# Optimization experiments

Hardware: AMD Instinct MI355X
Metric: run time of the kernel (lower is better)

The kernel has to match this reference:

```python
import jax, jax.numpy as jnp
import numpy as np

DEPTH = 7  # complete binary trees with 2**DEPTH = 128 leaves

B, L = 4096, 128
V, E, OUT = 100000, 128, 3


def setup_inputs() -> dict:
    key = jax.random.key(0)
    ks = jax.random.split(key, 6)
    tokens = jax.random.randint(ks[0], (B, L), 0, V, dtype=jnp.int64)
    embedding = jax.random.normal(ks[1], (V, E), dtype=jnp.float32)
    # tree_layer: Linear(2E -> E); torch stores weight as [out, in]
    W_tree = jax.random.normal(ks[2], (E, 2 * E), dtype=jnp.float32) * (1.0 / np.sqrt(2 * E))
    b_tree = jax.random.normal(ks[3], (E,), dtype=jnp.float32) * 0.01
    # classifier_layer: Linear(E -> OUT)
    W_cls = jax.random.normal(ks[4], (OUT, E), dtype=jnp.float32) * (1.0 / np.sqrt(E))
    b_cls = jax.random.normal(ks[5], (OUT,), dtype=jnp.float32) * 0.01
    return {"tokens": tokens, "embedding": embedding, "W_tree": W_tree,
            "b_tree": b_tree, "W_cls": W_cls, "b_cls": b_cls}


def reference(tokens, embedding, W_tree, b_tree, W_cls, b_cls):
    # Leaf embeddings: gather rows of the embedding table. [B, L, E]
    reps = embedding[tokens]
    # Level-synchronous bottom-up composition (depth-batched across all trees):
    # at each level, pair adjacent nodes, concat features, apply tree_layer + tanh.
    for _ in range(DEPTH):
        left = reps[:, 0::2, :]   # [B, n/2, E]
        right = reps[:, 1::2, :]  # [B, n/2, E]
        combined = jnp.concatenate([left, right], axis=-1)  # [B, n/2, 2E]
        reps = jnp.tanh(jnp.einsum('bnh,eh->bne', combined, W_tree) + b_tree)
    roots = reps[:, 0, :]  # [B, E]
    return roots @ W_cls.T + b_cls  # [B, OUT]
```

## Files before the change

### kernel.cpp

```cpp
#include <hip/hip_runtime.h>
#include <hip/hip_fp16.h>


typedef _Float16 half8 __attribute__((ext_vector_type(8)));
typedef float floatx4 __attribute__((ext_vector_type(4)));

#define STRIDE 264
#define UROW   33
#define NPAIR  2048

__device__ __forceinline__ float fast_tanh(float x) {
  float e = __expf(2.f * x);
  return 1.f - 2.f * __builtin_amdgcn_rcpf(e + 1.f);
}

__device__ __forceinline__ unsigned pkrtz(float a, float b) {
  auto h = __builtin_amdgcn_cvt_pkrtz(a, b);
  return __builtin_bit_cast(unsigned, h);
}

__device__ __forceinline__ void load16(const float* __restrict__ emb, int tok, int seg,
                                       float4 (&st)[16]) {
  const float4* src = (const float4*)emb + (size_t)tok * 32 + (seg & 1) * 16;
#pragma unroll
  for (int j = 0; j < 16; ++j) st[j] = src[j];
}
__device__ __forceinline__ void cvt_write(const float4 (&st)[16], _Float16* buf,
                                          int row, int seg) {
  uint4* dst = (uint4*)buf + row * UROW + seg * 8;
#pragma unroll
  for (int j = 0; j < 8; ++j) {
    float4 x = st[2 * j], y = st[2 * j + 1];
    uint4 w;
    w.x = pkrtz(x.x, x.y); w.y = pkrtz(x.z, x.w);
    w.z = pkrtz(y.x, y.y); w.w = pkrtz(y.z, y.w);
    dst[j] = w;
  }
}

__device__ __forceinline__ void mfma_k256(const _Float16* arow, const half8 (&Wf)[2][8],
                                          const float (&bias)[2], floatx4 (&accO)[2]) {
  floatx4 aA[2], aB[2];
#pragma unroll
  for (int i = 0; i < 2; ++i) {
    aA[i] = (floatx4){bias[i], bias[i], bias[i], bias[i]};
    aB[i] = (floatx4){0.f, 0.f, 0.f, 0.f};
  }
#pragma unroll
  for (int ks = 0; ks < 4; ++ks) {
    half8 x0 = *(const half8*)(arow + ks * 32);
    half8 x1 = *(const half8*)(arow + (ks + 4) * 32);
    aA[0] = __builtin_amdgcn_mfma_f32_16x16x32_f16(x0, Wf[0][ks],     aA[0], 0, 0, 0);
    aB[0] = __builtin_amdgcn_mfma_f32_16x16x32_f16(x1, Wf[0][ks + 4], aB[0], 0, 0, 0);
    aA[1] = __builtin_amdgcn_mfma_f32_16x16x32_f16(x0, Wf[1][ks],     aA[1], 0, 0, 0);
    aB[1] = __builtin_amdgcn_mfma_f32_16x16x32_f16(x1, Wf[1][ks + 4], aB[1], 0, 0, 0);
  }
  accO[0] = aA[0] + aB[0];
  accO[1] = aA[1] + aB[1];
}

template<int MT, int IN_S, int MVALID>
__device__ __forceinline__ void level_b(const _Float16* inb, _Float16* outb,
                                        const half8 (&Wf)[2][8], const float (&bias)[2],
                                        int nbase, int l15, int quad)
{
#pragma unroll
  for (int m = 0; m < MT; ++m) {
    floatx4 acc[2];
    mfma_k256(inb + (m * 16 + l15) * STRIDE + quad * 8, Wf, bias, acc);
    const int mrow = m * 16 + quad * 4;
#pragma unroll
    for (int i = 0; i < 2; ++i) {
      const int col = (nbase + i) * 16 + l15;
#pragma unroll
      for (int r = 0; r < 4; ++r) {
        const int node = mrow + r;
        if (MVALID == MT * 16 || node < MVALID) {
          const int s  = node / IN_S;
          const int ln = node % IN_S;
          float v = fast_tanh(acc[i][r]);
          outb[((ln >> 1) + s * (IN_S >> 1)) * STRIDE + (ln & 1) * 128 + col] = (_Float16)v;
        }
      }
    }
  }
}

__global__ __launch_bounds__(256, 2)
void tree_kernel(const int* __restrict__ tokens,
                 const float* __restrict__ embedding,
                 const float* __restrict__ W_tree,
                 const float* __restrict__ b_tree,
                 const float* __restrict__ W_cls,
                 const float* __restrict__ b_cls,
                 float* __restrict__ out)
{
  __shared__ __align__(16) _Float16 bufA[64 * STRIDE];
  __shared__ __align__(16) _Float16 bufB[32 * STRIDE];
  __shared__ __align__(16) _Float16 bufD[32 * STRIDE];
  __shared__ float wavepart[4][2][3];

  const int tid  = threadIdx.x;
  const int wid  = tid >> 6;
  const int lane = tid & 63;
  const int l15  = lane & 15;
  const int quad = lane >> 4;
  const int nbase = wid * 2;
  const int row  = tid & 63;
  const int seg  = tid >> 6;
  const int tidx = 2 * row + (seg >> 1);

  half8 Wf[2][8];
#pragma unroll
  for (int i = 0; i < 2; ++i) {
    const int e = (nbase + i) * 16 + l15;
#pragma unroll
    for (int ks = 0; ks < 8; ++ks) {
      const int k = ks * 32 + quad * 8;
      const float4* p = (const float4*)(W_tree + e * 256 + k);
      float4 lo = p[0], hi = p[1];
      half8 f;
      f[0] = (_Float16)lo.x; f[1] = (_Float16)lo.y; f[2] = (_Float16)lo.z; f[3] = (_Float16)lo.w;
      f[4] = (_Float16)hi.x; f[5] = (_Float16)hi.y; f[6] = (_Float16)hi.z; f[7] = (_Float16)hi.w;
      Wf[i][ks] = f;
    }
  }
  float bias[2];
#pragma unroll
  for (int i = 0; i < 2; ++i) bias[i] = b_tree[(nbase + i) * 16 + l15];

  float wc[2][3];
#pragma unroll
  for (int i = 0; i < 2; ++i) {
#pragma unroll
    for (int o = 0; o < 3; ++o) wc[i][o] = W_cls[o * 128 + (nbase + i) * 16 + l15];
  }

  int tokB_cur = tokens[(2 * blockIdx.x + 1) * 128 + tidx];
  {
    const int tokA0 = tokens[(2 * blockIdx.x) * 128 + tidx];
    float4 st[16];
    load16(embedding, tokA0, seg, st);
    cvt_write(st, bufA, row, seg);
  }
  __syncthreads();

#pragma unroll 1
  for (int p = blockIdx.x; p < NPAIR; p += gridDim.x) {
    int pn = p + gridDim.x;
    if (pn >= NPAIR) pn = p;
    const bool first = (p == (int)blockIdx.x);
    const int pprev = p - (int)gridDim.x;
    const int tokA_nxt = tokens[(2 * pn) * 128 + tidx];
    const int tokB_nxt = tokens[(2 * pn + 1) * 128 + tidx];

    if (!first) {
      floatx4 acc[2];
      mfma_k256(bufD + l15 * STRIDE + quad * 8, Wf, bias, acc);
      float part[2][3] = {{0.f, 0.f, 0.f}, {0.f, 0.f, 0.f}};
      if (quad == 0) {
#pragma unroll
        for (int i = 0; i < 2; ++i)
#pragma unroll
          for (int rr = 0; rr < 2; ++rr) {
            float v = fast_tanh(acc[i][rr]);
#pragma unroll
            for (int o = 0; o < 3; ++o) part[rr][o] = fmaf(v, wc[i][o], part[rr][o]);
          }
      }
#pragma unroll
      for (int rr = 0; rr < 2; ++rr)
#pragma unroll
        for (int o = 0; o < 3; ++o) {
          float v = part[rr][o];
          v += __shfl_down(v, 8);
          v += __shfl_down(v, 4);
          v += __shfl_down(v, 2);
          v += __shfl_down(v, 1);
          if (lane == 0) wavepart[wid][rr][o] = v;
        }
    }
    level_b<4, 64, 64>(bufA, bufB, Wf, bias, nbase, l15, quad);
    __syncthreads();

    {
      float4 st[16];
      load16(embedding, tokB_cur, seg, st);
      if (!first && tid < 6) {
        const int rr = tid / 3, o = tid - 3 * rr;
        float v = wavepart[0][rr][o] + wavepart[1][rr][o]
                + wavepart[2][rr][o] + wavepart[3][rr][o];
        out[(2 * pprev + rr) * 3 + o] = v + b_cls[o];
      }
      level_b<2, 32, 32>(bufB, bufD, Wf, bias, nbase, l15, quad);
      cvt_write(st, bufA, row, seg);
    }
    __syncthreads();

    level_b<4, 64, 64>(bufA, bufB, Wf, bias, nbase, l15, quad);
    __syncthreads();

    {
      float4 st[16];
      load16(embedding, tokA_nxt, seg, st);
      level_b<2, 32, 32>(bufB, bufD + 16 * STRIDE, Wf, bias, nbase, l15, quad);
      cvt_write(st, bufA, row, seg);
    }
    __syncthreads();

    level_b<2, 16, 32>(bufD, bufB, Wf, bias, nbase, l15, quad);
    __syncthreads();

    level_b<1, 8, 16>(bufB, bufD, Wf, bias, nbase, l15, quad);
    __syncthreads();

    level_b<1, 4, 8>(bufD, bufB, Wf, bias, nbase, l15, quad);
    __syncthreads();

    level_b<1, 2, 4>(bufB, bufD, Wf, bias, nbase, l15, quad);
    __syncthreads();

    tokB_cur = tokB_nxt;
  }

  {
    const int plast = (int)blockIdx.x + ((NPAIR / 1 - 1 - (int)blockIdx.x) / (int)gridDim.x) * (int)gridDim.x;
    floatx4 acc[2];
    mfma_k256(bufD + l15 * STRIDE + quad * 8, Wf, bias, acc);
    float part[2][3] = {{0.f, 0.f, 0.f}, {0.f, 0.f, 0.f}};
    if (quad == 0) {
#pragma unroll
      for (int i = 0; i < 2; ++i)
#pragma unroll
        for (int rr = 0; rr < 2; ++rr) {
          float v = fast_tanh(acc[i][rr]);
#pragma unroll
          for (int o = 0; o < 3; ++o) part[rr][o] = fmaf(v, wc[i][o], part[rr][o]);
        }
    }
#pragma unroll
    for (int rr = 0; rr < 2; ++rr)
#pragma unroll
      for (int o = 0; o < 3; ++o) {
        float v = part[rr][o];
        v += __shfl_down(v, 8);
        v += __shfl_down(v, 4);
        v += __shfl_down(v, 2);
        v += __shfl_down(v, 1);
        if (lane == 0) wavepart[wid][rr][o] = v;
      }
    __syncthreads();
    if (tid < 6) {
      const int rr = tid / 3, o = tid - 3 * rr;
      float v = wavepart[0][rr][o] + wavepart[1][rr][o]
              + wavepart[2][rr][o] + wavepart[3][rr][o];
      out[(2 * plast + rr) * 3 + o] = v + b_cls[o];
    }
  }
}

extern "C" void kernel_launch(void* const* d_in, const int* in_sizes, int n_in,
                              void* d_out, int out_size, void* d_ws, size_t ws_size,
                              hipStream_t stream) {
  const int*   tokens    = (const int*)d_in[0];
  const float* embedding = (const float*)d_in[1];
  const float* W_tree    = (const float*)d_in[2];
  const float* b_tree    = (const float*)d_in[3];
  const float* W_cls     = (const float*)d_in[4];
  const float* b_cls     = (const float*)d_in[5];
  float* out = (float*)d_out;

  dim3 grid(512), block(256);
  tree_kernel<<<grid, block, 0, stream>>>(tokens, embedding, W_tree, b_tree, W_cls, b_cls, out);
}
```

Before: 164.0 us.

## Double block size to 8 waves splitting M tiles across two wave groups

Grows the block from 4 to 8 waves. The two groups of 4 waves split the row (M) tiles of each tree level, and the embedding gather is spread over twice as many threads in smaller chunks. The root/classifier step runs on the second group while the first group starts the next level. Classifier weights are now loaded on demand rather than held in registers. The goal is more latency hiding and lower per-wave register pressure. The cost is idle waves in the deep levels, where only group 0 works, and launch bounds that may force register spills.

After: 209.6 us. +27.8%, slower.

```diff
diff --git a/kernel.cpp b/kernel.cpp
--- a/kernel.cpp
+++ b/kernel.cpp
@@ -19,17 +19,17 @@
   return __builtin_bit_cast(unsigned, h);
 }
 
-__device__ __forceinline__ void load16(const float* __restrict__ emb, int tok, int seg,
-                                       float4 (&st)[16]) {
-  const float4* src = (const float4*)emb + (size_t)tok * 32 + (seg & 1) * 16;
-#pragma unroll
-  for (int j = 0; j < 16; ++j) st[j] = src[j];
-}
-__device__ __forceinline__ void cvt_write(const float4 (&st)[16], _Float16* buf,
-                                          int row, int seg) {
-  uint4* dst = (uint4*)buf + row * UROW + seg * 8;
-#pragma unroll
-  for (int j = 0; j < 8; ++j) {
+__device__ __forceinline__ void load4(const float* __restrict__ emb, int tok, int seg,
+                                      int b, float4 (&st)[4]) {
+  const float4* src = (const float4*)emb + (size_t)tok * 32 + (seg & 3) * 8 + b * 4;
+#pragma unroll
+  for (int j = 0; j < 4; ++j) st[j] = src[j];
+}
+__device__ __forceinline__ void cvt_write4(const float4 (&st)[4], _Float16* buf,
+                                           int row, int seg, int b) {
+  uint4* dst = (uint4*)buf + row * UROW + (seg >> 2) * 16 + (seg & 3) * 4 + b * 2;
+#pragma unroll
+  for (int j = 0; j < 2; ++j) {
     float4 x = st[2 * j], y = st[2 * j + 1];
     uint4 w;
     w.x = pkrtz(x.x, x.y); w.y = pkrtz(x.z, x.w);
@@ -59,23 +59,23 @@
   accO[1] = aA[1] + aB[1];
 }
 
-template<int MT, int IN_S, int MVALID>
+template<int MT_LOC, int IN_S, int MVALID>
 __device__ __forceinline__ void level_b(const _Float16* inb, _Float16* outb,
                                         const half8 (&Wf)[2][8], const float (&bias)[2],
-                                        int nbase, int l15, int quad)
+                                        int mbase, int nbase, int l15, int quad)
 {
 #pragma unroll
-  for (int m = 0; m < MT; ++m) {
+  for (int m = 0; m < MT_LOC; ++m) {
     floatx4 acc[2];
-    mfma_k256(inb + (m * 16 + l15) * STRIDE + quad * 8, Wf, bias, acc);
-    const int mrow = m * 16 + quad * 4;
+    mfma_k256(inb + ((mbase + m) * 16 + l15) * STRIDE + quad * 8, Wf, bias, acc);
+    const int mrow = (mbase + m) * 16 + quad * 4;
 #pragma unroll
     for (int i = 0; i < 2; ++i) {
       const int col = (nbase + i) * 16 + l15;
 #pragma unroll
       for (int r = 0; r < 4; ++r) {
         const int node = mrow + r;
-        if (MVALID == MT * 16 || node < MVALID) {
+        if (MVALID < 0 || node < MVALID) {
           const int s  = node / IN_S;
           const int ln = node % IN_S;
           float v = fast_tanh(acc[i][r]);
@@ -86,7 +86,7 @@
   }
 }
 
-__global__ __launch_bounds__(256, 2)
+__global__ __launch_bounds__(512, 4)
 void tree_kernel(const int* __restrict__ tokens,
                  const float* __restrict__ embedding,
                  const float* __restrict__ W_tree,
@@ -105,10 +105,12 @@
   const int lane = tid & 63;
   const int l15  = lane & 15;
   const int quad = lane >> 4;
-  const int nbase = wid * 2;
+  const int wn   = wid & 3;
+  const int wm   = wid >> 2;
+  const int nbase = wn * 2;
   const int row  = tid & 63;
   const int seg  = tid >> 6;
-  const int tidx = 2 * row + (seg >> 1);
+  const int tidx = 2 * row + (seg >> 2);
 
   half8 Wf[2][8];
 #pragma unroll
@@ -129,24 +131,19 @@
 #pragma unroll
   for (int i = 0; i < 2; ++i) bias[i] = b_tree[(nbase + i) * 16 + l15];
 
-  float wc[2][3];
-#pragma unroll
-  for (int i = 0; i < 2; ++i) {
-#pragma unroll
-    for (int o = 0; o < 3; ++o) wc[i][o] = W_cls[o * 128 + (nbase + i) * 16 + l15];
-  }
-
   int tokB_cur = tokens[(2 * blockIdx.x + 1) * 128 + tidx];
   {
     const int tokA0 = tokens[(2 * blockIdx.x) * 128 + tidx];
-    float4 st[16];
-    load16(embedding, tokA0, seg, st);
-    cvt_write(st, bufA, row, seg);
+    float4 st0[4], st1[4];
+    load4(embedding, tokA0, seg, 0, st0);
+    load4(embedding, tokA0, seg, 1, st1);
+    cvt_write4(st0, bufA, row, seg, 0);
+    cvt_write4(st1, bufA, row, seg, 1);
   }
   __syncthreads();
 
 #pragma unroll 1
-  for (int p = blockIdx.x; p < NPAIR; p += gridDim.x) {
+  for (int p = blockIdx.x; p < NPAIR; p += (int)gridDim.x) {
     int pn = p + gridDim.x;
     if (pn >= NPAIR) pn = p;
     const bool first = (p == (int)blockIdx.x);
@@ -154,18 +151,114 @@
     const int tokA_nxt = tokens[(2 * pn) * 128 + tidx];
     const int tokB_nxt = tokens[(2 * pn + 1) * 128 + tidx];
 
-    if (!first) {
+    if (wm == 1) {
+      if (!first) {
+        floatx4 acc[2];
+        mfma_k256(bufD + l15 * STRIDE + quad * 8, Wf, bias, acc);
+        float part[2][3] = {{0.f, 0.f, 0.f}, {0.f, 0.f, 0.f}};
+        if (quad == 0) {
+          float wcl[2][3];
+#pragma unroll
+          for (int i = 0; i < 2; ++i)
+#pragma unroll
+            for (int o = 0; o < 3; ++o) wcl[i][o] = W_cls[o * 128 + (nbase + i) * 16 + l15];
+#pragma unroll
+          for (int i = 0; i < 2; ++i)
+#pragma unroll
+            for (int rr = 0; rr < 2; ++rr) {
+              float v = fast_tanh(acc[i][rr]);
+#pragma unroll
+              for (int o = 0; o < 3; ++o) part[rr][o] = fmaf(v, wcl[i][o], part[rr][o]);
+            }
+        }
+#pragma unroll
+        for (int rr = 0; rr < 2; ++rr)
+#pragma unroll
+          for (int o = 0; o < 3; ++o) {
+            float v = part[rr][o];
+            v += __shfl_down(v, 8);
+            v += __shfl_down(v, 4);
+            v += __shfl_down(v, 2);
+            v += __shfl_down(v, 1);
+            if (lane == 0) wavepart[wn][rr][o] = v;
+          }
+      }
+      level_b<2, 64, -1>(bufA, bufB, Wf, bias, 2, nbase, l15, quad);
+    } else {
+      level_b<2, 64, -1>(bufA, bufB, Wf, bias, 0, nbase, l15, quad);
+    }
+    __syncthreads();
+
+    {
+      float4 st0[4];
+      load4(embedding, tokB_cur, seg, 0, st0);
+      __builtin_amdgcn_sched_barrier(0);
+      if (!first && tid < 6) {
+        const int rr = tid / 3, o = tid - 3 * rr;
+        float v = wavepart[0][rr][o] + wavepart[1][rr][o]
+                + wavepart[2][rr][o] + wavepart[3][rr][o];
+        out[(2 * pprev + rr) * 3 + o] = v + b_cls[o];
+      }
+      level_b<1, 32, -1>(bufB, bufD, Wf, bias, wm, nbase, l15, quad);
+      __builtin_amdgcn_sched_barrier(0);
+      float4 st1[4];
+      load4(embedding, tokB_cur, seg, 1, st1);
+      cvt_write4(st0, bufA, row, seg, 0);
+      cvt_write4(st1, bufA, row, seg, 1);
+    }
+    __syncthreads();
+
+    level_b<2, 64, -1>(bufA, bufB, Wf, bias, wm * 2, nbase, l15, quad);
+    __syncthreads();
+
+    {
+      float4 st0[4];
+      load4(embedding, tokA_nxt, seg, 0, st0);
+      __builtin_amdgcn_sched_barrier(0);
+      level_b<1, 32, -1>(bufB, bufD + 16 * STRIDE, Wf, bias, wm, nbase, l15, quad);
+      __builtin_amdgcn_sched_barrier(0);
+      float4 st1[4];
+      load4(embedding, tokA_nxt, seg, 1, st1);
+      cvt_write4(st0, bufA, row, seg, 0);
+      cvt_write4(st1, bufA, row, seg, 1);
+    }
+    __syncthreads();
+
+    level_b<1, 16, -1>(bufD, bufB, Wf, bias, wm, nbase, l15, quad);
+    __syncthreads();
+
+    if (wm == 0) level_b<1, 8, -1>(bufB, bufD, Wf, bias, 0, nbase, l15, quad);
+    __syncthreads();
+
+    if (wm == 0) level_b<1, 4, 8>(bufD, bufB, Wf, bias, 0, nbase, l15, quad);
+    __syncthreads();
+
+    if (wm == 0) level_b<1, 2, 4>(bufB, bufD, Wf, bias, 0, nbase, l15, quad);
+    __syncthreads();
+
+    tokB_cur = tokB_nxt;
+  }
+
+  {
+    const int plast = (int)blockIdx.x
+        + ((NPAIR - 1 - (int)blockIdx.x) / (int)gridDim.x) * (int)gridDim.x;
+    if (wm == 1) {
       floatx4 acc[2];
       mfma_k256(bufD + l15 * STRIDE + quad * 8, Wf, bias, acc);
       float part[2][3] = {{0.f, 0.f, 0.f}, {0.f, 0.f, 0.f}};
       if (quad == 0) {
+        float wcl[2][3];
+#pragma unroll
+        for (int i = 0; i < 2; ++i)
+#pragma unroll
+          for (int o = 0; o < 3; ++o) wcl[i][o] = W_cls[o * 128 + (nbase + i) * 16 + l15];
 #pragma unroll
         for (int i = 0; i < 2; ++i)
 #pragma unroll
           for (int rr = 0; rr < 2; ++rr) {
             float v = fast_tanh(acc[i][rr]);
 #pragma unroll
-            for (int o = 0; o < 3; ++o) part[rr][o] = fmaf(v, wc[i][o], part[rr][o]);
+            for (int o = 0; o < 3; ++o) part[rr][o] = fmaf(v, wcl[i][o], part[rr][o]);
           }
       }
 #pragma unroll
@@ -177,78 +270,9 @@
           v += __shfl_down(v, 4);
           v += __shfl_down(v, 2);
           v += __shfl_down(v, 1);
-          if (lane == 0) wavepart[wid][rr][o] = v;
+          if (lane == 0) wavepart[wn][rr][o] = v;
         }
     }
-    level_b<4, 64, 64>(bufA, bufB, Wf, bias, nbase, l15, quad);
-    __syncthreads();
-
-    {
-      float4 st[16];
-      load16(embedding, tokB_cur, seg, st);
-      if (!first && tid < 6) {
-        const int rr = tid / 3, o = tid - 3 * rr;
-        float v = wavepart[0][rr][o] + wavepart[1][rr][o]
-                + wavepart[2][rr][o] + wavepart[3][rr][o];
-        out[(2 * pprev + rr) * 3 + o] = v + b_cls[o];
-      }
-      level_b<2, 32, 32>(bufB, bufD, Wf, bias, nbase, l15, quad);
-      cvt_write(st, bufA, row, seg);
-    }
-    __syncthreads();
-
-    level_b<4, 64, 64>(bufA, bufB, Wf, bias, nbase, l15, quad);
-    __syncthreads();
-
-    {
-      float4 st[16];
-      load16(embedding, tokA_nxt, seg, st);
-      level_b<2, 32, 32>(bufB, bufD + 16 * STRIDE, Wf, bias, nbase, l15, quad);
-      cvt_write(st, bufA, row, seg);
-    }
-    __syncthreads();
-
-    level_b<2, 16, 32>(bufD, bufB, Wf, bias, nbase, l15, quad);
-    __syncthreads();
-
-    level_b<1, 8, 16>(bufB, bufD, Wf, bias, nbase, l15, quad);
-    __syncthreads();
-
-    level_b<1, 4, 8>(bufD, bufB, Wf, bias, nbase, l15, quad);
-    __syncthreads();
-
-    level_b<1, 2, 4>(bufB, bufD, Wf, bias, nbase, l15, quad);
-    __syncthreads();
-
-    tokB_cur = tokB_nxt;
-  }
-
-  {
-    const int plast = (int)blockIdx.x + ((NPAIR / 1 - 1 - (int)blockIdx.x) / (int)gridDim.x) * (int)gridDim.x;
-    floatx4 acc[2];
-    mfma_k256(bufD + l15 * STRIDE + quad * 8, Wf, bias, acc);
-    float part[2][3] = {{0.f, 0.f, 0.f}, {0.f, 0.f, 0.f}};
-    if (quad == 0) {
-#pragma unroll
-      for (int i = 0; i < 2; ++i)
-#pragma unroll
-        for (int rr = 0; rr < 2; ++rr) {
-          float v = fast_tanh(acc[i][rr]);
-#pragma unroll
-          for (int o = 0; o < 3; ++o) part[rr][o] = fmaf(v, wc[i][o], part[rr][o]);
-        }
-    }
-#pragma unroll
-    for (int rr = 0; rr < 2; ++rr)
-#pragma unroll
-      for (int o = 0; o < 3; ++o) {
-        float v = part[rr][o];
-        v += __shfl_down(v, 8);
-        v += __shfl_down(v, 4);
-        v += __shfl_down(v, 2);
-        v += __shfl_down(v, 1);
-        if (lane == 0) wavepart[wid][rr][o] = v;
-      }
     __syncthreads();
     if (tid < 6) {
       const int rr = tid / 3, o = tid - 3 * rr;
@@ -270,6 +294,6 @@
   const float* b_cls     = (const float*)d_in[5];
   float* out = (float*)d_out;
 
-  dim3 grid(512), block(256);
+  dim3 grid(512), block(512);
   tree_kernel<<<grid, block, 0, stream>>>(tokens, embedding, W_tree, b_tree, W_cls, b_cls, out);
 }
```

## Shrink LDS buffers and halve embedding staging to fit three blocks per CU

Applied to the files above, without the earlier changes.

Replaces the 32-row bufD with a 6-row bufC and restructures the level schedule so both trees of a pair reuse bufA/bufB in place. Embedding loads are split into two 8-float4 halves per thread, which cuts register staging. The classifier weights are now loaded only when used. Together these let launch bounds rise to 3 blocks per CU and the grid grow to 768, trading more barriers and extra level steps for higher occupancy and more latency hiding.

Result: slower. 183.1 us (+11.6%).

```diff
diff --git a/kernel.cpp b/kernel.cpp
--- a/kernel.cpp
+++ b/kernel.cpp
@@ -19,17 +19,17 @@
   return __builtin_bit_cast(unsigned, h);
 }
 
-__device__ __forceinline__ void load16(const float* __restrict__ emb, int tok, int seg,
-                                       float4 (&st)[16]) {
-  const float4* src = (const float4*)emb + (size_t)tok * 32 + (seg & 1) * 16;
-#pragma unroll
-  for (int j = 0; j < 16; ++j) st[j] = src[j];
-}
-__device__ __forceinline__ void cvt_write(const float4 (&st)[16], _Float16* buf,
-                                          int row, int seg) {
-  uint4* dst = (uint4*)buf + row * UROW + seg * 8;
-#pragma unroll
-  for (int j = 0; j < 8; ++j) {
+__device__ __forceinline__ void load8(const float* __restrict__ emb, int tok, int q,
+                                      float4 (&st)[8]) {
+  const float4* src = (const float4*)emb + (size_t)tok * 32 + q * 8;
+#pragma unroll
+  for (int j = 0; j < 8; ++j) st[j] = src[j];
+}
+__device__ __forceinline__ void cvt_write8(const float4 (&st)[8], _Float16* buf,
+                                           int row, int lb, int q) {
+  uint4* dst = (uint4*)buf + row * UROW + lb * 16 + q * 4;
+#pragma unroll
+  for (int j = 0; j < 4; ++j) {
     float4 x = st[2 * j], y = st[2 * j + 1];
     uint4 w;
     w.x = pkrtz(x.x, x.y); w.y = pkrtz(x.z, x.w);
@@ -75,7 +75,7 @@
 #pragma unroll
       for (int r = 0; r < 4; ++r) {
         const int node = mrow + r;
-        if (MVALID == MT * 16 || node < MVALID) {
+        if (MVALID < 0 || node < MVALID) {
           const int s  = node / IN_S;
           const int ln = node % IN_S;
           float v = fast_tanh(acc[i][r]);
@@ -86,7 +86,7 @@
   }
 }
 
-__global__ __launch_bounds__(256, 2)
+__global__ __launch_bounds__(256, 3)
 void tree_kernel(const int* __restrict__ tokens,
                  const float* __restrict__ embedding,
                  const float* __restrict__ W_tree,
@@ -97,7 +97,7 @@
 {
   __shared__ __align__(16) _Float16 bufA[64 * STRIDE];
   __shared__ __align__(16) _Float16 bufB[32 * STRIDE];
-  __shared__ __align__(16) _Float16 bufD[32 * STRIDE];
+  __shared__ __align__(16) _Float16 bufC[6 * STRIDE];
   __shared__ float wavepart[4][2][3];
 
   const int tid  = threadIdx.x;
@@ -106,9 +106,10 @@
   const int l15  = lane & 15;
   const int quad = lane >> 4;
   const int nbase = wid * 2;
-  const int row  = tid & 63;
-  const int seg  = tid >> 6;
-  const int tidx = 2 * row + (seg >> 1);
+  const int gr   = tid & 31;
+  const int glb  = (tid >> 7) & 1;
+  const int gq   = (tid >> 5) & 3;
+  const int li   = 2 * gr + glb;
 
   half8 Wf[2][8];
 #pragma unroll
@@ -129,43 +130,67 @@
 #pragma unroll
   for (int i = 0; i < 2; ++i) bias[i] = b_tree[(nbase + i) * 16 + l15];
 
-  float wc[2][3];
-#pragma unroll
-  for (int i = 0; i < 2; ++i) {
-#pragma unroll
-    for (int o = 0; o < 3; ++o) wc[i][o] = W_cls[o * 128 + (nbase + i) * 16 + l15];
-  }
-
-  int tokB_cur = tokens[(2 * blockIdx.x + 1) * 128 + tidx];
+  int tokS1lo = tokens[(2 * blockIdx.x + 1) * 128 + li];
+  int tokS1hi = tokens[(2 * blockIdx.x + 1) * 128 + 64 + li];
   {
-    const int tokA0 = tokens[(2 * blockIdx.x) * 128 + tidx];
-    float4 st[16];
-    load16(embedding, tokA0, seg, st);
-    cvt_write(st, bufA, row, seg);
+    const int tlo = tokens[(2 * blockIdx.x) * 128 + li];
+    const int thi = tokens[(2 * blockIdx.x) * 128 + 64 + li];
+    float4 st[8];
+    load8(embedding, tlo, gq, st);
+    cvt_write8(st, bufA, gr, glb, gq);
+    load8(embedding, thi, gq, st);
+    cvt_write8(st, bufA, 32 + gr, glb, gq);
   }
   __syncthreads();
 
 #pragma unroll 1
-  for (int p = blockIdx.x; p < NPAIR; p += gridDim.x) {
+  for (int p = blockIdx.x; p < NPAIR; p += (int)gridDim.x) {
     int pn = p + gridDim.x;
     if (pn >= NPAIR) pn = p;
     const bool first = (p == (int)blockIdx.x);
     const int pprev = p - (int)gridDim.x;
-    const int tokA_nxt = tokens[(2 * pn) * 128 + tidx];
-    const int tokB_nxt = tokens[(2 * pn + 1) * 128 + tidx];
+    const int tokN0lo = tokens[(2 * pn) * 128 + li];
+    const int tokN0hi = tokens[(2 * pn) * 128 + 64 + li];
 
     if (!first) {
+      const int rc = l15 < 4 ? l15 : 3;
       floatx4 acc[2];
-      mfma_k256(bufD + l15 * STRIDE + quad * 8, Wf, bias, acc);
+      mfma_k256(bufC + rc * STRIDE + quad * 8, Wf, bias, acc);
+      const int mrow = quad * 4;
+#pragma unroll
+      for (int i = 0; i < 2; ++i) {
+        const int col = (nbase + i) * 16 + l15;
+#pragma unroll
+        for (int r = 0; r < 4; ++r) {
+          const int node = mrow + r;
+          if (node < 4) {
+            float v = fast_tanh(acc[i][r]);
+            bufC[(4 + (node >> 1)) * STRIDE + (node & 1) * 128 + col] = (_Float16)v;
+          }
+        }
+      }
+    }
+    level_b<4, 64, -1>(bufA, bufB, Wf, bias, nbase, l15, quad);
+    __syncthreads();
+
+    if (!first) {
+      const int rc = 4 + (l15 < 2 ? l15 : 1);
+      floatx4 acc[2];
+      mfma_k256(bufC + rc * STRIDE + quad * 8, Wf, bias, acc);
       float part[2][3] = {{0.f, 0.f, 0.f}, {0.f, 0.f, 0.f}};
       if (quad == 0) {
+        float wcl[2][3];
+#pragma unroll
+        for (int i = 0; i < 2; ++i)
+#pragma unroll
+          for (int o = 0; o < 3; ++o) wcl[i][o] = W_cls[o * 128 + (nbase + i) * 16 + l15];
 #pragma unroll
         for (int i = 0; i < 2; ++i)
 #pragma unroll
           for (int rr = 0; rr < 2; ++rr) {
             float v = fast_tanh(acc[i][rr]);
 #pragma unroll
-            for (int o = 0; o < 3; ++o) part[rr][o] = fmaf(v, wc[i][o], part[rr][o]);
+            for (int o = 0; o < 3; ++o) part[rr][o] = fmaf(v, wcl[i][o], part[rr][o]);
           }
       }
 #pragma unroll
@@ -180,75 +205,117 @@
           if (lane == 0) wavepart[wid][rr][o] = v;
         }
     }
-    level_b<4, 64, 64>(bufA, bufB, Wf, bias, nbase, l15, quad);
-    __syncthreads();
-
-    {
-      float4 st[16];
-      load16(embedding, tokB_cur, seg, st);
+    level_b<2, 32, -1>(bufB, bufA, Wf, bias, nbase, l15, quad);
+    __syncthreads();
+
+    {
+      float4 st[8];
+      load8(embedding, tokS1hi, gq, st);
       if (!first && tid < 6) {
         const int rr = tid / 3, o = tid - 3 * rr;
         float v = wavepart[0][rr][o] + wavepart[1][rr][o]
                 + wavepart[2][rr][o] + wavepart[3][rr][o];
         out[(2 * pprev + rr) * 3 + o] = v + b_cls[o];
       }
-      level_b<2, 32, 32>(bufB, bufD, Wf, bias, nbase, l15, quad);
-      cvt_write(st, bufA, row, seg);
-    }
-    __syncthreads();
-
-    level_b<4, 64, 64>(bufA, bufB, Wf, bias, nbase, l15, quad);
-    __syncthreads();
-
-    {
-      float4 st[16];
-      load16(embedding, tokA_nxt, seg, st);
-      level_b<2, 32, 32>(bufB, bufD + 16 * STRIDE, Wf, bias, nbase, l15, quad);
-      cvt_write(st, bufA, row, seg);
-    }
-    __syncthreads();
-
-    level_b<2, 16, 32>(bufD, bufB, Wf, bias, nbase, l15, quad);
-    __syncthreads();
-
-    level_b<1, 8, 16>(bufB, bufD, Wf, bias, nbase, l15, quad);
-    __syncthreads();
-
-    level_b<1, 4, 8>(bufD, bufB, Wf, bias, nbase, l15, quad);
-    __syncthreads();
-
-    level_b<1, 2, 4>(bufB, bufD, Wf, bias, nbase, l15, quad);
-    __syncthreads();
-
-    tokB_cur = tokB_nxt;
+      level_b<1, 16, -1>(bufA, bufB, Wf, bias, nbase, l15, quad);
+      cvt_write8(st, bufA, 32 + gr, glb, gq);
+    }
+    __syncthreads();
+
+    {
+      float4 st[8];
+      load8(embedding, tokS1lo, gq, st);
+      level_b<1, 8, 8>(bufB, bufB + 16 * STRIDE, Wf, bias, nbase, l15, quad);
+      cvt_write8(st, bufA, gr, glb, gq);
+    }
+    __syncthreads();
+
+    level_b<1, 4, 4>(bufB + 16 * STRIDE, bufC, Wf, bias, nbase, l15, quad);
+    __syncthreads();
+
+    level_b<4, 64, -1>(bufA, bufB, Wf, bias, nbase, l15, quad);
+    __syncthreads();
+
+    {
+      float4 st[8];
+      load8(embedding, tokN0hi, gq, st);
+      level_b<2, 32, -1>(bufB, bufA, Wf, bias, nbase, l15, quad);
+      cvt_write8(st, bufA, 32 + gr, glb, gq);
+    }
+    __syncthreads();
+
+    level_b<1, 16, -1>(bufA, bufB, Wf, bias, nbase, l15, quad);
+    __syncthreads();
+
+    {
+      float4 st[8];
+      load8(embedding, tokN0lo, gq, st);
+      level_b<1, 8, 8>(bufB, bufB + 16 * STRIDE, Wf, bias, nbase, l15, quad);
+      cvt_write8(st, bufA, gr, glb, gq);
+    }
+    __syncthreads();
+
+    level_b<1, 4, 4>(bufB + 16 * STRIDE, bufC + 2 * STRIDE, Wf, bias, nbase, l15, quad);
+    __syncthreads();
+
+    tokS1lo = tokens[(2 * pn + 1) * 128 + li];
+    tokS1hi = tokens[(2 * pn + 1) * 128 + 64 + li];
   }
 
   {
-    const int plast = (int)blockIdx.x + ((NPAIR / 1 - 1 - (int)blockIdx.x) / (int)gridDim.x) * (int)gridDim.x;
-    floatx4 acc[2];
-    mfma_k256(bufD + l15 * STRIDE + quad * 8, Wf, bias, acc);
-    float part[2][3] = {{0.f, 0.f, 0.f}, {0.f, 0.f, 0.f}};
-    if (quad == 0) {
-#pragma unroll
-      for (int i = 0; i < 2; ++i)
-#pragma unroll
-        for (int rr = 0; rr < 2; ++rr) {
-          float v = fast_tanh(acc[i][rr]);
-#pragma unroll
-          for (int o = 0; o < 3; ++o) part[rr][o] = fmaf(v, wc[i][o], part[rr][o]);
-        }
-    }
-#pragma unroll
-    for (int rr = 0; rr < 2; ++rr)
-#pragma unroll
-      for (int o = 0; o < 3; ++o) {
-        float v = part[rr][o];
-        v += __shfl_down(v, 8);
-        v += __shfl_down(v, 4);
-        v += __shfl_down(v, 2);
-        v += __shfl_down(v, 1);
-        if (lane == 0) wavepart[wid][rr][o] = v;
-      }
+    const int plast = (int)blockIdx.x
+        + ((NPAIR - 1 - (int)blockIdx.x) / (int)gridDim.x) * (int)gridDim.x;
+    {
+      const int rc = l15 < 4 ? l15 : 3;
+      floatx4 acc[2];
+      mfma_k256(bufC + rc * STRIDE + quad * 8, Wf, bias, acc);
+      const int mrow = quad * 4;
+#pragma unroll
+      for (int i = 0; i < 2; ++i) {
+        const int col = (nbase + i) * 16 + l15;
+#pragma unroll
+        for (int r = 0; r < 4; ++r) {
+          const int node = mrow + r;
+          if (node < 4) {
+            float v = fast_tanh(acc[i][r]);
+            bufC[(4 + (node >> 1)) * STRIDE + (node & 1) * 128 + col] = (_Float16)v;
+          }
+        }
+      }
+    }
+    __syncthreads();
+    {
+      const int rc = 4 + (l15 < 2 ? l15 : 1);
+      floatx4 acc[2];
+      mfma_k256(bufC + rc * STRIDE + quad * 8, Wf, bias, acc);
+      float part[2][3] = {{0.f, 0.f, 0.f}, {0.f, 0.f, 0.f}};
+      if (quad == 0) {
+        float wcl[2][3];
+#pragma unroll
+        for (int i = 0; i < 2; ++i)
+#pragma unroll
+          for (int o = 0; o < 3; ++o) wcl[i][o] = W_cls[o * 128 + (nbase + i) * 16 + l15];
+#pragma unroll
+        for (int i = 0; i < 2; ++i)
+#pragma unroll
+          for (int rr = 0; rr < 2; ++rr) {
+            float v = fast_tanh(acc[i][rr]);
+#pragma unroll
+            for (int o = 0; o < 3; ++o) part[rr][o] = fmaf(v, wcl[i][o], part[rr][o]);
+          }
+      }
+#pragma unroll
+      for (int rr = 0; rr < 2; ++rr)
+#pragma unroll
+        for (int o = 0; o < 3; ++o) {
+          float v = part[rr][o];
+          v += __shfl_down(v, 8);
+          v += __shfl_down(v, 4);
+          v += __shfl_down(v, 2);
+          v += __shfl_down(v, 1);
+          if (lane == 0) wavepart[wid][rr][o] = v;
+        }
+    }
     __syncthreads();
     if (tid < 6) {
       const int rr = tid / 3, o = tid - 3 * rr;
@@ -270,6 +337,6 @@
   const float* b_cls     = (const float*)d_in[5];
   float* out = (float*)d_out;
 
-  dim3 grid(512), block(256);
+  dim3 grid(768), block(256);
   tree_kernel<<<grid, block, 0, stream>>>(tokens, embedding, W_tree, b_tree, W_cls, b_cls, out);
 }
```
